# Performance work log

Hardware: AMD Instinct MI355X
Metric: run time of the kernel (lower is better)

The kernel has to match this reference:

```python
import jax, jax.numpy as jnp
import numpy as np

B, T, D, H = 512, 200, 128, 128


def setup_inputs() -> dict:
    key = jax.random.key(0)
    ks = jax.random.split(key, 16)
    r = lambda k, shp, s=0.05: jax.random.normal(k, shp, dtype=jnp.float32) * s
    F = 3 * D + H  # concat([item_eb, his_sum, item_eb*his_sum, final_state2])
    return {
        "item_eb": jax.random.normal(ks[0], (B, D), dtype=jnp.float32),
        "item_his_eb": jax.random.normal(ks[1], (B, T, D), dtype=jnp.float32),
        "Wg1": r(ks[2], (D + H, 2 * H)), "bg1": jnp.ones((2 * H,), jnp.float32),
        "Wc1": r(ks[3], (D + H, H)), "bc1": jnp.zeros((H,), jnp.float32),
        "att_w1": r(ks[4], (4 * H, 80)), "att_b1": jnp.zeros((80,), jnp.float32),
        "att_w2": r(ks[5], (80, 40)), "att_b2": jnp.zeros((40,), jnp.float32),
        "att_w3": r(ks[6], (40, 1)), "att_b3": jnp.zeros((1,), jnp.float32),
        "Wg2": r(ks[7], (2 * H, 2 * H)), "bg2": jnp.ones((2 * H,), jnp.float32),
        "Wc2": r(ks[8], (2 * H, H)), "bc2": jnp.zeros((H,), jnp.float32),
        "fc1_w": r(ks[9], (F, 200)), "fc1_b": jnp.zeros((200,), jnp.float32),
        "alpha1": jnp.full((200,), 0.25, jnp.float32),
        "fc2_w": r(ks[10], (200, 80)), "fc2_b": jnp.zeros((80,), jnp.float32),
        "alpha2": jnp.full((80,), 0.25, jnp.float32),
        "fc3_w": r(ks[11], (80, 2)), "fc3_b": jnp.zeros((2,), jnp.float32),
        "seq_len": jax.random.randint(ks[12], (B,), 1, T + 1).astype(jnp.int32),
    }


def _gru_scan(x_btd, Wg, bg, Wc, bc, seq_len, att=None):
    """GRU (TF GRUCell math) or AUGRU if att [B,T] is given.
    Honors sequence_length semantics of tf dynamic_rnn: state copied through,
    outputs zeroed past each row's length."""
    Bx, Tx, _ = x_btd.shape
    Hh = Wc.shape[1]
    xs = jnp.swapaxes(x_btd, 0, 1)  # [T,B,Din]
    ts = jnp.arange(Tx)
    a_ts = jnp.swapaxes(att, 0, 1) if att is not None else jnp.zeros((Tx, Bx), x_btd.dtype)
    h0 = jnp.zeros((Bx, Hh), x_btd.dtype)

    def step(h, xat):
        x, a, t = xat
        gates = jax.nn.sigmoid(jnp.concatenate([x, h], axis=-1) @ Wg + bg)
        rg, u = jnp.split(gates, 2, axis=-1)
        c = jnp.tanh(jnp.concatenate([x, rg * h], axis=-1) @ Wc + bc)
        if att is not None:  # VecAttGRUCell: u = (1 - att_score) * u
            u = (1.0 - a[:, None]) * u
        hn = u * h + (1.0 - u) * c
        valid = (t < seq_len)[:, None]
        hn = jnp.where(valid, hn, h)
        out = jnp.where(valid, hn, jnp.zeros_like(hn))
        return hn, out

    hT, outs = jax.lax.scan(step, h0, (xs, a_ts, ts))
    return jnp.swapaxes(outs, 0, 1), hT  # [B,T,H], [B,H]


def _forward(item_eb, item_his_eb, Wg1, bg1, Wc1, bc1, att_w1, att_b1, att_w2, att_b2,
             att_w3, att_b3, Wg2, bg2, Wc2, bc2, fc1_w, fc1_b, alpha1, fc2_w, fc2_b,
             alpha2, fc3_w, fc3_b, seq_len):
    Bx, Tx, Dx = item_his_eb.shape
    mask = jnp.arange(Tx)[None, :] < seq_len[:, None]  # [B,T] bool
    # rnn_1: plain GRU over history embeddings
    rnn1, _ = _gru_scan(item_his_eb, Wg1, bg1, Wc1, bc1, seq_len)
    # din_fcn_attention: concat trick + 3-layer scorer + masked softmax
    q = jnp.broadcast_to(item_eb[:, None, :], rnn1.shape)
    din_all = jnp.concatenate([q, rnn1, q - rnn1, q * rnn1], axis=-1)  # [B,T,4H]
    h1 = jax.nn.sigmoid(din_all @ att_w1 + att_b1)
    h2 = jax.nn.sigmoid(h1 @ att_w2 + att_b2)
    scores = (h2 @ att_w3 + att_b3)[..., 0]  # [B,T]
    NEG_INF = jnp.float32(-(2.0 ** 32) + 1.0)  # DIEN padding value
    scores = jnp.where(mask, scores, NEG_INF)
    alphas = jax.nn.softmax(scores, axis=-1)  # [B,T]
    # rnn_2: AUGRU (VecAttGRUCell) gated by attention scores; take final state
    _, final_state2 = _gru_scan(rnn1, Wg2, bg2, Wc2, bc2, seq_len, att=alphas)
    # fcn head on concatenated features
    his_sum = jnp.sum(item_his_eb * mask[..., None].astype(item_his_eb.dtype), axis=1)
    feat = jnp.concatenate([item_eb, his_sum, item_eb * his_sum, final_state2], axis=-1)
    prelu = lambda x, a: jnp.maximum(x, 0.0) + a * jnp.minimum(x, 0.0)
    z = prelu(feat @ fc1_w + fc1_b, alpha1)
    z = prelu(z @ fc2_w + fc2_b, alpha2)
    logits = z @ fc3_w + fc3_b  # [B,2]
    return jax.nn.softmax(logits, axis=-1)


def reference(item_eb, item_his_eb, Wg1, bg1, Wc1, bc1, att_w1, att_b1, att_w2, att_b2,
              att_w3, att_b3, Wg2, bg2, Wc2, bc2, fc1_w, fc1_b, alpha1, fc2_w, fc2_b,
              alpha2, fc3_w, fc3_b, seq_len):
    return _forward(item_eb, item_his_eb, Wg1, bg1, Wc1, bc1, att_w1, att_b1, att_w2,
                    att_b2, att_w3, att_b3, Wg2, bg2, Wc2, bc2, fc1_w, fc1_b, alpha1,
                    fc2_w, fc2_b, alpha2, fc3_w, fc3_b, seq_len)
```

## Files before the change

kernel.cpp:

```cpp
#include <hip/hip_runtime.h>
#include <hip/hip_bf16.h>


typedef __attribute__((ext_vector_type(8))) short bf16x8;
typedef __attribute__((ext_vector_type(4))) float f32x4;
typedef _Float16 f16x2 __attribute__((ext_vector_type(2)));

#define NC 4
#define TC 50

static __device__ __forceinline__ unsigned short f2bf(float f) {
  union { __hip_bfloat16 h; unsigned short u; } v;
  v.h = __float2bfloat16(f);
  return v.u;
}
static __device__ __forceinline__ float bf2f(unsigned short u) {
  union { __hip_bfloat16 h; unsigned short u; } v;
  v.u = u;
  return __bfloat162float(v.h);
}
static __device__ __forceinline__ unsigned short f2h(float f) {
  union { _Float16 h; unsigned short u; } v;
  v.h = (_Float16)f;
  return v.u;
}
static __device__ __forceinline__ unsigned int pkf16(float a, float b) {
  union { f16x2 v; unsigned int u; } c;
  c.v = (f16x2){(_Float16)a, (_Float16)b};
  return c.u;
}
static __device__ __forceinline__ float dot2f(unsigned int w, unsigned int h, float acc) {
  union { unsigned int u; f16x2 v; } a, b;
  a.u = w; b.u = h;
#if __has_builtin(__builtin_amdgcn_fdot2)
  return __builtin_amdgcn_fdot2(a.v, b.v, acc, false);
#else
  return acc + (float)a.v.x * (float)b.v.x + (float)a.v.y * (float)b.v.y;
#endif
}

__global__ __launch_bounds__(256) void prep_weights(
    const float* __restrict__ Wg1, const float* __restrict__ Wc1,
    const float* __restrict__ Wg2, const float* __restrict__ Wc2,
    const float* __restrict__ aw1, const float* __restrict__ aw2,
    const float* __restrict__ bg1, const float* __restrict__ bc1,
    const float* __restrict__ bg2, const float* __restrict__ bc2,
    const float* __restrict__ ab1, const float* __restrict__ ab2,
    unsigned short* __restrict__ W1xT, unsigned short* __restrict__ W2xT,
    unsigned short* __restrict__ AW1T, unsigned short* __restrict__ AW2T,
    float* __restrict__ b384_1, float* __restrict__ b384_2,
    float* __restrict__ bA1, float* __restrict__ bA2,
    unsigned int* __restrict__ WgP1, unsigned int* __restrict__ WcP1,
    unsigned int* __restrict__ WgP2, unsigned int* __restrict__ WcP2)
{
  int e = blockIdx.x * 256 + threadIdx.x;
  if (e < 49152) {
    int n = e >> 7, k = e & 127;
    float v1 = (n < 256) ? Wg1[k * 256 + n] : Wc1[k * 128 + (n - 256)];
    float v2 = (n < 256) ? Wg2[k * 256 + n] : Wc2[k * 128 + (n - 256)];
    W1xT[e] = f2bf(v1);
    W2xT[e] = f2bf(v2);
  }
  if (e < 65536) {
    int n = e >> 9, k = e & 511;
    AW1T[e] = f2bf(n < 80 ? aw1[k * 80 + n] : 0.f);
  }
  if (e < 16384) {
    int n = e >> 7, k = e & 127;
    AW2T[e] = f2bf((n < 40 && k < 80) ? aw2[k * 40 + n] : 0.f);
  }
  if (e < 16384) {
    int i = e >> 8, tt = e & 255;
    int row = 128 + 2 * i;
    WgP1[e] = pkf16(Wg1[row * 256 + tt], Wg1[(row + 1) * 256 + tt]);
    WgP2[e] = pkf16(Wg2[row * 256 + tt], Wg2[(row + 1) * 256 + tt]);
  }
  if (e < 8192) {
    int i = e >> 8, tt = e & 255;
    int jc = tt >> 1, half = tt & 1;
    int row = 128 + half * 64 + 2 * i;
    WcP1[e] = pkf16(Wc1[row * 128 + jc], Wc1[(row + 1) * 128 + jc]);
    WcP2[e] = pkf16(Wc2[row * 128 + jc], Wc2[(row + 1) * 128 + jc]);
  }
  if (e < 384) {
    b384_1[e] = (e < 256) ? bg1[e] : bc1[e - 256];
    b384_2[e] = (e < 256) ? bg2[e] : bc2[e - 256];
  }
  if (e < 128) {
    bA1[e] = (e < 80) ? ab1[e] : 0.f;
    bA2[e] = (e < 40) ? ab2[e] : 0.f;
  }
}

__global__ __launch_bounds__(256) void zero_f(float* __restrict__ p, int n) {
  int i = blockIdx.x * 256 + threadIdx.x;
  if (i < n) p[i] = 0.f;
}

__global__ __launch_bounds__(256) void cast_his_t(const float4* __restrict__ in4,
                                                  ushort4* __restrict__ out4)
{
  int i = blockIdx.x * 256 + threadIdx.x;
  float4 v = in4[i];
  int d4 = (i & 31) << 2;
  int bt = i >> 5;
  int tt = bt % 200, bb = bt / 200;
  out4[(((size_t)tt * 512 + bb) * 128 + d4) >> 2] =
      make_ushort4(f2bf(v.x), f2bf(v.y), f2bf(v.z), f2bf(v.w));
}

template <int EPI>
__global__ __launch_bounds__(256) void gemm_bt(
    const unsigned short* __restrict__ A, const unsigned short* __restrict__ BT,
    const float* __restrict__ bias, float* __restrict__ Cf,
    unsigned short* __restrict__ Cb, int K, int ldc)
{
  __shared__ uint4 AsB[1024];
  __shared__ uint4 BsB[1024];
  const int tid = threadIdx.x;
  const int w = tid >> 6, l = tid & 63;
  const long mBase = (long)blockIdx.x * 128;
  const int nBase = blockIdx.y * 128;

  f32x4 acc[2][8];
#pragma unroll
  for (int m = 0; m < 2; m++)
#pragma unroll
    for (int n = 0; n < 8; n++) acc[m][n] = 0.f;

  const int srow = (tid >> 3) & 31;
  const int scc = l & 7;

  for (int kb = 0; kb < K; kb += 64) {
#pragma unroll
    for (int p = 0; p < 4; p++) {
      int row = p * 32 + srow;
      uint4 va = *(const uint4*)(A + (size_t)(mBase + row) * K + kb + scc * 8);
      uint4 vb = *(const uint4*)(BT + (size_t)(nBase + row) * K + kb + scc * 8);
      AsB[row * 8 + (scc ^ (row & 7))] = va;
      BsB[row * 8 + (scc ^ (row & 7))] = vb;
    }
    __syncthreads();
#pragma unroll
    for (int ks = 0; ks < 2; ks++) {
      int ccr = ks * 4 + (l >> 4);
      int r0 = w * 32 + (l & 15);
      int r1 = r0 + 16;
      bf16x8 a0 = *(const bf16x8*)&AsB[r0 * 8 + (ccr ^ (r0 & 7))];
      bf16x8 a1 = *(const bf16x8*)&AsB[r1 * 8 + (ccr ^ (r1 & 7))];
#pragma unroll
      for (int n = 0; n < 8; n++) {
        int rb = n * 16 + (l & 15);
        bf16x8 bn = *(const bf16x8*)&BsB[rb * 8 + (ccr ^ (rb & 7))];
        acc[0][n] = __builtin_amdgcn_mfma_f32_16x16x32_bf16(a0, bn, acc[0][n], 0, 0, 0);
        acc[1][n] = __builtin_amdgcn_mfma_f32_16x16x32_bf16(a1, bn, acc[1][n], 0, 0, 0);
      }
    }
    __syncthreads();
  }

  const int lcol = l & 15, lrow4 = (l >> 4) * 4;
#pragma unroll
  for (int n = 0; n < 8; n++) {
    int gcol = nBase + n * 16 + lcol;
    float bb = bias[gcol];
#pragma unroll
    for (int m = 0; m < 2; m++) {
#pragma unroll
      for (int i = 0; i < 4; i++) {
        long grow = mBase + w * 32 + m * 16 + lrow4 + i;
        float v = acc[m][n][i] + bb;
        if (EPI == 0) {
          Cf[grow * ldc + gcol] = v;
        } else if (EPI == 1) {
          Cb[grow * ldc + gcol] = f2bf(1.f / (1.f + __expf(-v)));
        } else {
          Cb[grow * ldc + gcol] = f2h(v);
        }
      }
    }
  }
}

template <int AUGRU>
__global__ __launch_bounds__(256, 3) void gru_chunk(
    const unsigned short* __restrict__ xproj,
    const unsigned int* __restrict__ WgP,
    const unsigned int* __restrict__ WcP,
    const int* __restrict__ seqlen,
    const float* __restrict__ alphas,
    unsigned short* __restrict__ outbf,
    float* __restrict__ hstate,
    int tbase)
{
  const int t = threadIdx.x;
  const int r = blockIdx.x;
  const int jc = t >> 1, half = t & 1;
  const int len = seqlen[r];
  int nsteps = len - tbase;
  if (nsteps > TC) nsteps = TC;

  if (nsteps <= 0) {
    if (!AUGRU) {
      for (int s = 0; s < TC; s++) {
        unsigned int* zp = (unsigned int*)(outbf + ((size_t)(tbase + s) * 512 + r) * 128);
        if (t < 64) zp[t] = 0;
      }
    }
    return;
  }

  unsigned int wg[64], wc[32];
#pragma unroll
  for (int i = 0; i < 64; i++) wg[i] = WgP[i * 256 + t];
#pragma unroll
  for (int i = 0; i < 32; i++) wc[i] = WcP[i * 256 + t];

  __shared__ float hF[128];
  __shared__ float uF[128];
  __shared__ unsigned int hH[64];
  __shared__ unsigned int rghP[64];

  if (t < 128) hF[t] = hstate[r * 128 + t];
  if (t < 64) hH[t] = pkf16(hstate[r * 128 + 2 * t], hstate[r * 128 + 2 * t + 1]);
  __syncthreads();

  const _Float16* xp = (const _Float16*)xproj;
  const size_t rowStride = (size_t)512 * 384;
  float xg = (float)xp[(size_t)r * 384 + t];
  float xc = (float)xp[(size_t)r * 384 + 256 + jc];
  float al = AUGRU ? alphas[r * 200 + tbase] : 0.f;

  for (int ts = 0; ts < nsteps; ++ts) {
    float a0 = 0.f, a1 = 0.f, a2 = 0.f, a3 = 0.f;
#pragma unroll
    for (int q = 0; q < 4; q++) {
      uint4 h0 = *(const uint4*)&hH[q * 16 + 0];
      uint4 h1 = *(const uint4*)&hH[q * 16 + 4];
      uint4 h2 = *(const uint4*)&hH[q * 16 + 8];
      uint4 h3 = *(const uint4*)&hH[q * 16 + 12];
      a0 = dot2f(wg[q * 16 + 0], h0.x, a0);  a1 = dot2f(wg[q * 16 + 1], h0.y, a1);
      a2 = dot2f(wg[q * 16 + 2], h0.z, a2);  a3 = dot2f(wg[q * 16 + 3], h0.w, a3);
      a0 = dot2f(wg[q * 16 + 4], h1.x, a0);  a1 = dot2f(wg[q * 16 + 5], h1.y, a1);
      a2 = dot2f(wg[q * 16 + 6], h1.z, a2);  a3 = dot2f(wg[q * 16 + 7], h1.w, a3);
      a0 = dot2f(wg[q * 16 + 8], h2.x, a0);  a1 = dot2f(wg[q * 16 + 9], h2.y, a1);
      a2 = dot2f(wg[q * 16 + 10], h2.z, a2); a3 = dot2f(wg[q * 16 + 11], h2.w, a3);
      a0 = dot2f(wg[q * 16 + 12], h3.x, a0); a1 = dot2f(wg[q * 16 + 13], h3.y, a1);
      a2 = dot2f(wg[q * 16 + 14], h3.z, a2); a3 = dot2f(wg[q * 16 + 15], h3.w, a3);
    }
    float a = (a0 + a1) + (a2 + a3) + xg;
    float g = 1.f / (1.f + __expf(-a));
    float rgh = 0.f;
    if (t < 128) rgh = g * hF[t];
    float rh2 = __shfl_down(rgh, 1);
    if (t < 128) {
      if ((t & 1) == 0) rghP[t >> 1] = pkf16(rgh, rh2);
    } else {
      uF[t - 128] = g;
    }
    int tsn = (ts + 1 < nsteps) ? ts + 1 : nsteps - 1;
    float xg_n = (float)xp[(size_t)tsn * rowStride + (size_t)r * 384 + t];
    float xc_n = (float)xp[(size_t)tsn * rowStride + (size_t)r * 384 + 256 + jc];
    float al_n = AUGRU ? alphas[r * 200 + tbase + tsn] : 0.f;
    __syncthreads();

    float c0 = 0.f, c1 = 0.f;
    const uint4* rp = (const uint4*)&rghP[half * 32];
#pragma unroll
    for (int q = 0; q < 8; q++) {
      uint4 rq = rp[q];
      c0 = dot2f(wc[q * 4 + 0], rq.x, c0);
      c1 = dot2f(wc[q * 4 + 1], rq.y, c1);
      c0 = dot2f(wc[q * 4 + 2], rq.z, c0);
      c1 = dot2f(wc[q * 4 + 3], rq.w, c1);
    }
    float c = c0 + c1;
    c += __shfl_xor(c, 1);
    c += xc;
    c = fminf(fmaxf(c, -15.f), 15.f);
    float e2 = __expf(2.f * c);
    c = 1.f - 2.f / (e2 + 1.f);
    float u = uF[jc];
    if (AUGRU) u *= (1.f - al);
    float h = hF[jc];
    float hn = u * h + (1.f - u) * c;
    float hnHi = __shfl_down(hn, 2);
    if ((t & 1) == 0) {
      hF[jc] = hn;
      if (!AUGRU) outbf[((size_t)(tbase + ts) * 512 + r) * 128 + jc] = f2bf(hn);
    }
    if ((t & 3) == 0) hH[t >> 2] = pkf16(hn, hnHi);
    __syncthreads();

    xg = xg_n; xc = xc_n; al = al_n;
  }

  if (t < 128) hstate[r * 128 + t] = hF[t];
  if (!AUGRU && nsteps < TC) {
    for (int s = nsteps; s < TC; s++) {
      unsigned int* zp = (unsigned int*)(outbf + ((size_t)(tbase + s) * 512 + r) * 128);
      if (t < 64) zp[t] = 0;
    }
  }
}

__global__ __launch_bounds__(256) void build_din(
    const float* __restrict__ item_eb, const unsigned short* __restrict__ rnn1bf,
    ushort4* __restrict__ din, int rowbase)
{
  int i = blockIdx.x * 256 + threadIdx.x;
  int r = i >> 5;
  int d4 = (i & 31) << 2;
  int b = r & 511;
  float4 q = *(const float4*)(item_eb + b * 128 + d4);
  const unsigned short* rp = rnn1bf + ((size_t)rowbase + r) * 128 + d4;
  unsigned short s0 = rp[0], s1 = rp[1], s2 = rp[2], s3 = rp[3];
  float r0 = bf2f(s0), r1 = bf2f(s1), r2 = bf2f(s2), r3 = bf2f(s3);
  size_t base = (size_t)r * 512 + d4;
  din[(base + 0) >> 2]   = make_ushort4(f2bf(q.x), f2bf(q.y), f2bf(q.z), f2bf(q.w));
  din[(base + 128) >> 2] = make_ushort4(s0, s1, s2, s3);
  din[(base + 256) >> 2] = make_ushort4(f2bf(q.x - r0), f2bf(q.y - r1), f2bf(q.z - r2), f2bf(q.w - r3));
  din[(base + 384) >> 2] = make_ushort4(f2bf(q.x * r0), f2bf(q.y * r1), f2bf(q.z * r2), f2bf(q.w * r3));
}

__global__ __launch_bounds__(256) void scorer(
    const unsigned short* __restrict__ h2, const float* __restrict__ w3,
    const float* __restrict__ b3, float* __restrict__ scores, int tbase)
{
  int r = blockIdx.x * 256 + threadIdx.x;
  int b = r & 511, tp = r >> 9;
  const unsigned short* row = h2 + (size_t)r * 128;
  float acc = b3[0];
#pragma unroll 8
  for (int k = 0; k < 40; k++) acc += bf2f(row[k]) * w3[k];
  scores[b * 200 + tbase + tp] = acc;
}

__global__ __launch_bounds__(256) void mask_softmax(
    const float* __restrict__ scores, const int* __restrict__ seqlen,
    float* __restrict__ alphas)
{
  int b = blockIdx.x, t = threadIdx.x;
  __shared__ float red[256];
  int len = seqlen[b];
  float s = (t < 200 && t < len) ? scores[b * 200 + t] : -1e30f;
  red[t] = s;
  __syncthreads();
  for (int o = 128; o > 0; o >>= 1) {
    if (t < o) red[t] = fmaxf(red[t], red[t + o]);
    __syncthreads();
  }
  float m = red[0];
  __syncthreads();
  float e = (t < 200 && t < len) ? __expf(s - m) : 0.f;
  red[t] = e;
  __syncthreads();
  for (int o = 128; o > 0; o >>= 1) {
    if (t < o) red[t] += red[t + o];
    __syncthreads();
  }
  float denom = red[0];
  if (t < 200) alphas[b * 200 + t] = e / denom;
}

__global__ __launch_bounds__(128) void feat_kernel(
    const float* __restrict__ item_eb, const float* __restrict__ his,
    const int* __restrict__ seqlen, const float* __restrict__ hT,
    float* __restrict__ feat)
{
  int b = blockIdx.x, d = threadIdx.x;
  int len = seqlen[b];
  float s = 0.f;
  const float* hp = his + (size_t)b * 200 * 128 + d;
  for (int ts = 0; ts < len; ++ts) s += hp[ts * 128];
  float q = item_eb[b * 128 + d];
  feat[b * 512 + d] = q;
  feat[b * 512 + 128 + d] = s;
  feat[b * 512 + 256 + d] = q * s;
  feat[b * 512 + 384 + d] = hT[b * 128 + d];
}

__global__ __launch_bounds__(256) void head_kernel(
    const float* __restrict__ feat,
    const float* __restrict__ w1, const float* __restrict__ b1, const float* __restrict__ a1,
    const float* __restrict__ w2, const float* __restrict__ b2, const float* __restrict__ a2,
    const float* __restrict__ w3, const float* __restrict__ b3,
    float* __restrict__ out)
{
  int b = blockIdx.x, t = threadIdx.x;
  __shared__ float frow[512];
  __shared__ float z1[200];
  __shared__ float z2[80];
  frow[t] = feat[b * 512 + t];
  frow[256 + t] = feat[b * 512 + 256 + t];
  __syncthreads();
  if (t < 200) {
    float acc = b1[t];
#pragma unroll 8
    for (int k = 0; k < 512; k++) acc += frow[k] * w1[k * 200 + t];
    z1[t] = acc > 0.f ? acc : a1[t] * acc;
  }
  __syncthreads();
  if (t < 80) {
    float acc = b2[t];
#pragma unroll 8
    for (int k = 0; k < 200; k++) acc += z1[k] * w2[k * 80 + t];
    z2[t] = acc > 0.f ? acc : a2[t] * acc;
  }
  __syncthreads();
  if (t == 0) {
    float l0 = b3[0], l1 = b3[1];
    for (int k = 0; k < 80; k++) {
      float z = z2[k];
      l0 += z * w3[k * 2];
      l1 += z * w3[k * 2 + 1];
    }
    float m = fmaxf(l0, l1);
    float e0 = __expf(l0 - m), e1 = __expf(l1 - m);
    out[b * 2 + 0] = e0 / (e0 + e1);
    out[b * 2 + 1] = e1 / (e0 + e1);
  }
}

extern "C" void kernel_launch(void* const* d_in, const int* in_sizes, int n_in,
                              void* d_out, int out_size, void* d_ws, size_t ws_size,
                              hipStream_t stream)
{
  const float* item_eb = (const float*)d_in[0];
  const float* his     = (const float*)d_in[1];
  const float* Wg1     = (const float*)d_in[2];
  const float* bg1     = (const float*)d_in[3];
  const float* Wc1     = (const float*)d_in[4];
  const float* bc1     = (const float*)d_in[5];
  const float* aw1     = (const float*)d_in[6];
  const float* ab1     = (const float*)d_in[7];
  const float* aw2     = (const float*)d_in[8];
  const float* ab2     = (const float*)d_in[9];
  const float* aw3     = (const float*)d_in[10];
  const float* ab3     = (const float*)d_in[11];
  const float* Wg2     = (const float*)d_in[12];
  const float* bg2     = (const float*)d_in[13];
  const float* Wc2     = (const float*)d_in[14];
  const float* bc2     = (const float*)d_in[15];
  const float* fc1w    = (const float*)d_in[16];
  const float* fc1b    = (const float*)d_in[17];
  const float* al1     = (const float*)d_in[18];
  const float* fc2w    = (const float*)d_in[19];
  const float* fc2b    = (const float*)d_in[20];
  const float* al2     = (const float*)d_in[21];
  const float* fc3w    = (const float*)d_in[22];
  const float* fc3b    = (const float*)d_in[23];
  const int*   seqlen  = (const int*)d_in[24];

  char* ws = (char*)d_ws;
  unsigned short* XhA    = (unsigned short*)(ws + 0L);
  unsigned short* xprojC = (unsigned short*)(ws + 26214400L);
  unsigned short* h1C    = (unsigned short*)(ws + 26214400L);
  unsigned short* h2C    = (unsigned short*)(ws + 32768000L);
  unsigned short* rnn1   = (unsigned short*)(ws + 45875200L);
  float*          scores = (float*)(ws + 72089600L);
  float*          alphas = (float*)(ws + 72499200L);
  float*          hstate = (float*)(ws + 72908800L);
  float*          feat   = (float*)(ws + 73170944L);
  unsigned int*   WgP1   = (unsigned int*)(ws + 74219520L);
  unsigned int*   WcP1   = (unsigned int*)(ws + 74285056L);
  unsigned int*   WgP2   = (unsigned int*)(ws + 74317824L);
  unsigned int*   WcP2   = (unsigned int*)(ws + 74383360L);
  unsigned short* W1xT   = (unsigned short*)(ws + 74416128L);
  unsigned short* W2xT   = (unsigned short*)(ws + 74514432L);
  unsigned short* AW1T   = (unsigned short*)(ws + 74612736L);
  unsigned short* AW2T   = (unsigned short*)(ws + 74743808L);
  float*          b384_1 = (float*)(ws + 74776576L);
  float*          b384_2 = (float*)(ws + 74778112L);
  float*          bA1    = (float*)(ws + 74779648L);
  float*          bA2    = (float*)(ws + 74780160L);

  const size_t chunkRows = (size_t)TC * 512;

  prep_weights<<<256, 256, 0, stream>>>(Wg1, Wc1, Wg2, Wc2, aw1, aw2, bg1, bc1,
                                        bg2, bc2, ab1, ab2,
                                        W1xT, W2xT, AW1T, AW2T, b384_1, b384_2, bA1, bA2,
                                        WgP1, WcP1, WgP2, WcP2);
  cast_his_t<<<12800, 256, 0, stream>>>((const float4*)his, (ushort4*)XhA);
  zero_f<<<256, 256, 0, stream>>>(hstate, 65536);

  for (int c = 0; c < NC; c++) {
    gemm_bt<2><<<dim3(200, 3), 256, 0, stream>>>(XhA + c * chunkRows * 128, W1xT,
                                                 b384_1, nullptr, xprojC, 128, 384);
    gru_chunk<0><<<512, 256, 0, stream>>>(xprojC, WgP1, WcP1, seqlen, nullptr,
                                          rnn1, hstate, c * TC);
  }

  for (int c = 0; c < NC; c++) {
    build_din<<<3200, 256, 0, stream>>>(item_eb, rnn1, (ushort4*)XhA, (int)(c * chunkRows));
    gemm_bt<1><<<dim3(200, 1), 256, 0, stream>>>(XhA, AW1T, bA1, nullptr, h1C, 512, 128);
    gemm_bt<1><<<dim3(200, 1), 256, 0, stream>>>(h1C, AW2T, bA2, nullptr, h2C, 128, 128);
    scorer<<<100, 256, 0, stream>>>(h2C, aw3, ab3, scores, c * TC);
  }
  mask_softmax<<<512, 256, 0, stream>>>(scores, seqlen, alphas);

  zero_f<<<256, 256, 0, stream>>>(hstate, 65536);
  for (int c = 0; c < NC; c++) {
    gemm_bt<2><<<dim3(200, 3), 256, 0, stream>>>(rnn1 + c * chunkRows * 128, W2xT,
                                                 b384_2, nullptr, xprojC, 128, 384);
    gru_chunk<1><<<512, 256, 0, stream>>>(xprojC, WgP2, WcP2, seqlen, alphas,
                                          nullptr, hstate, c * TC);
  }

  feat_kernel<<<512, 128, 0, stream>>>(item_eb, his, seqlen, hstate, feat);
  head_kernel<<<512, 256, 0, stream>>>(feat, fc1w, fc1b, al1, fc2w, fc2b, al2,
                                       fc3w, fc3b, (float*)d_out);
}
```

Baseline: 744.2 us.

## Fuse GRU chunks with next-chunk projection and attention GEMMs in combined launches

```diff
diff --git a/kernel.cpp b/kernel.cpp
--- a/kernel.cpp
+++ b/kernel.cpp
@@ -8,6 +8,8 @@
 
 #define NC 4
 #define TC 50
+#define CROWS 25600
+#define CSH 3276800
 
 static __device__ __forceinline__ unsigned short f2bf(float f) {
   union { __hip_bfloat16 h; unsigned short u; } v;
@@ -24,25 +26,26 @@
   v.h = (_Float16)f;
   return v.u;
 }
+static __device__ __forceinline__ float h2f(unsigned short u) {
+  union { unsigned short u; _Float16 h; } v;
+  v.u = u;
+  return (float)v.h;
+}
 static __device__ __forceinline__ unsigned int pkf16(float a, float b) {
   union { f16x2 v; unsigned int u; } c;
   c.v = (f16x2){(_Float16)a, (_Float16)b};
   return c.u;
 }
-static __device__ __forceinline__ float dot2f(unsigned int w, unsigned int h, float acc) {
-  union { unsigned int u; f16x2 v; } a, b;
-  a.u = w; b.u = h;
-#if __has_builtin(__builtin_amdgcn_fdot2)
-  return __builtin_amdgcn_fdot2(a.v, b.v, acc, false);
-#else
-  return acc + (float)a.v.x * (float)b.v.x + (float)a.v.y * (float)b.v.y;
-#endif
+static __device__ __forceinline__ void dot2a(float& acc, unsigned int w, unsigned int h) {
+  asm volatile("v_dot2_f32_f16 %0, %1, %2, %0" : "+v"(acc) : "v"(w), "v"(h));
 }
 
 __global__ __launch_bounds__(256) void prep_weights(
+    const float* __restrict__ item_eb,
     const float* __restrict__ Wg1, const float* __restrict__ Wc1,
     const float* __restrict__ Wg2, const float* __restrict__ Wc2,
     const float* __restrict__ aw1, const float* __restrict__ aw2,
+    const float* __restrict__ aw3,
     const float* __restrict__ bg1, const float* __restrict__ bc1,
     const float* __restrict__ bg2, const float* __restrict__ bc2,
     const float* __restrict__ ab1, const float* __restrict__ ab2,
@@ -51,7 +54,9 @@
     float* __restrict__ b384_1, float* __restrict__ b384_2,
     float* __restrict__ bA1, float* __restrict__ bA2,
     unsigned int* __restrict__ WgP1, unsigned int* __restrict__ WcP1,
-    unsigned int* __restrict__ WgP2, unsigned int* __restrict__ WcP2)
+    unsigned int* __restrict__ WgP2, unsigned int* __restrict__ WcP2,
+    float* __restrict__ w3p, unsigned short* __restrict__ Xq,
+    float* __restrict__ hstate)
 {
   int e = blockIdx.x * 256 + threadIdx.x;
   if (e < 49152) {
@@ -64,6 +69,8 @@
   if (e < 65536) {
     int n = e >> 9, k = e & 511;
     AW1T[e] = f2bf(n < 80 ? aw1[k * 80 + n] : 0.f);
+    Xq[e] = f2bf(item_eb[e]);
+    hstate[e] = 0.f;
   }
   if (e < 16384) {
     int n = e >> 7, k = e & 127;
@@ -89,12 +96,8 @@
   if (e < 128) {
     bA1[e] = (e < 80) ? ab1[e] : 0.f;
     bA2[e] = (e < 40) ? ab2[e] : 0.f;
-  }
-}
-
-__global__ __launch_bounds__(256) void zero_f(float* __restrict__ p, int n) {
-  int i = blockIdx.x * 256 + threadIdx.x;
-  if (i < n) p[i] = 0.f;
+    w3p[e] = (e < 40) ? aw3[e] : 0.f;
+  }
 }
 
 __global__ __launch_bounds__(256) void cast_his_t(const float4* __restrict__ in4,
@@ -109,18 +112,42 @@
       make_ushort4(f2bf(v.x), f2bf(v.y), f2bf(v.z), f2bf(v.w));
 }
 
-template <int EPI>
-__global__ __launch_bounds__(256) void gemm_bt(
-    const unsigned short* __restrict__ A, const unsigned short* __restrict__ BT,
-    const float* __restrict__ bias, float* __restrict__ Cf,
-    unsigned short* __restrict__ Cb, int K, int ldc)
-{
-  __shared__ uint4 AsB[1024];
-  __shared__ uint4 BsB[1024];
+struct GemmP {
+  const unsigned short* A;
+  const unsigned short* B;
+  const float* bias;
+  unsigned short* out;
+  float* scores;
+  const float* w3p;
+  const float* b3;
+  const unsigned short* Xq;
+  const unsigned short* rnn1;
+  long rowbase;
+  int K, ldc, mtiles, tbase;
+};
+
+static __device__ __forceinline__ uint4 bfop(uint4 q, uint4 r, bool mul) {
+  unsigned short* qs = (unsigned short*)&q;
+  unsigned short* rs = (unsigned short*)&r;
+  uint4 o;
+  unsigned short* os = (unsigned short*)&o;
+#pragma unroll
+  for (int i = 0; i < 8; i++) {
+    float a = bf2f(qs[i]), b = bf2f(rs[i]);
+    os[i] = f2bf(mul ? a * b : a - b);
+  }
+  return o;
+}
+
+template <int SRC, int EPI>
+__device__ __forceinline__ void gemm_body(const GemmP& P, int tile, char* smem) {
+  uint4* AsB = (uint4*)smem;
+  uint4* BsB = AsB + 1024;
   const int tid = threadIdx.x;
   const int w = tid >> 6, l = tid & 63;
-  const long mBase = (long)blockIdx.x * 128;
-  const int nBase = blockIdx.y * 128;
+  const int mb = tile % P.mtiles, nb = tile / P.mtiles;
+  const long mBase = (long)mb * 128;
+  const int nBase = nb * 128;
 
   f32x4 acc[2][8];
 #pragma unroll
@@ -130,13 +157,31 @@
 
   const int srow = (tid >> 3) & 31;
   const int scc = l & 7;
-
-  for (int kb = 0; kb < K; kb += 64) {
+  const int KK = SRC ? 512 : P.K;
+
+  for (int kb = 0; kb < KK; kb += 64) {
 #pragma unroll
     for (int p = 0; p < 4; p++) {
       int row = p * 32 + srow;
-      uint4 va = *(const uint4*)(A + (size_t)(mBase + row) * K + kb + scc * 8);
-      uint4 vb = *(const uint4*)(BT + (size_t)(nBase + row) * K + kb + scc * 8);
+      long grow = mBase + row;
+      uint4 va;
+      if (SRC == 0) {
+        va = *(const uint4*)(P.A + (size_t)grow * KK + kb + scc * 8);
+      } else {
+        int seg = kb >> 7;
+        int c0 = (kb & 127) + scc * 8;
+        int b = (int)(grow & 511);
+        if (seg == 0) {
+          va = *(const uint4*)(P.Xq + b * 128 + c0);
+        } else if (seg == 1) {
+          va = *(const uint4*)(P.rnn1 + (size_t)(P.rowbase + grow) * 128 + c0);
+        } else {
+          uint4 vq = *(const uint4*)(P.Xq + b * 128 + c0);
+          uint4 vr = *(const uint4*)(P.rnn1 + (size_t)(P.rowbase + grow) * 128 + c0);
+          va = bfop(vq, vr, seg == 3);
+        }
+      }
+      uint4 vb = *(const uint4*)(P.B + (size_t)(nBase + row) * KK + kb + scc * 8);
       AsB[row * 8 + (scc ^ (row & 7))] = va;
       BsB[row * 8 + (scc ^ (row & 7))] = vb;
     }
@@ -160,78 +205,115 @@
   }
 
   const int lcol = l & 15, lrow4 = (l >> 4) * 4;
-#pragma unroll
-  for (int n = 0; n < 8; n++) {
-    int gcol = nBase + n * 16 + lcol;
-    float bb = bias[gcol];
-#pragma unroll
-    for (int m = 0; m < 2; m++) {
-#pragma unroll
-      for (int i = 0; i < 4; i++) {
-        long grow = mBase + w * 32 + m * 16 + lrow4 + i;
-        float v = acc[m][n][i] + bb;
-        if (EPI == 0) {
-          Cf[grow * ldc + gcol] = v;
-        } else if (EPI == 1) {
-          Cb[grow * ldc + gcol] = f2bf(1.f / (1.f + __expf(-v)));
-        } else {
-          Cb[grow * ldc + gcol] = f2h(v);
+  if (EPI == 2) {
+    float sp[2][4] = {{0.f, 0.f, 0.f, 0.f}, {0.f, 0.f, 0.f, 0.f}};
+#pragma unroll
+    for (int n = 0; n < 8; n++) {
+      int gcol = n * 16 + lcol;
+      float bb = P.bias[gcol];
+      float w3 = P.w3p[gcol];
+#pragma unroll
+      for (int m = 0; m < 2; m++)
+#pragma unroll
+        for (int i = 0; i < 4; i++) {
+          float v = acc[m][n][i] + bb;
+          sp[m][i] += w3 / (1.f + __expf(-v));
         }
-      }
-    }
-  }
-}
+    }
+#pragma unroll
+    for (int msk = 1; msk < 16; msk <<= 1)
+#pragma unroll
+      for (int m = 0; m < 2; m++)
+#pragma unroll
+        for (int i = 0; i < 4; i++) sp[m][i] += __shfl_xor(sp[m][i], msk);
+    float b3v = P.b3[0];
+    if (lcol == 0) {
+#pragma unroll
+      for (int m = 0; m < 2; m++)
+#pragma unroll
+        for (int i = 0; i < 4; i++) {
+          long grow = mBase + w * 32 + m * 16 + lrow4 + i;
+          int b = (int)(grow & 511);
+          int tp = (int)(grow >> 9) + P.tbase;
+          P.scores[b * 200 + tp] = sp[m][i] + b3v;
+        }
+    }
+  } else {
+#pragma unroll
+    for (int n = 0; n < 8; n++) {
+      int gcol = nBase + n * 16 + lcol;
+      float bb = P.bias[gcol];
+#pragma unroll
+      for (int m = 0; m < 2; m++)
+#pragma unroll
+        for (int i = 0; i < 4; i++) {
+          long grow = mBase + w * 32 + m * 16 + lrow4 + i;
+          float v = acc[m][n][i] + bb;
+          if (EPI == 0) P.out[grow * P.ldc + gcol] = f2h(v);
+          else          P.out[grow * P.ldc + gcol] = f2bf(1.f / (1.f + __expf(-v)));
+        }
+    }
+  }
+}
+
+struct GruP {
+  const unsigned short* xproj;
+  const unsigned int* WgP;
+  const unsigned int* WcP;
+  const int* seqlen;
+  const float* alphas;
+  unsigned short* outbf;
+  float* hstate;
+  int tbase;
+};
 
 template <int AUGRU>
-__global__ __launch_bounds__(256, 3) void gru_chunk(
-    const unsigned short* __restrict__ xproj,
-    const unsigned int* __restrict__ WgP,
-    const unsigned int* __restrict__ WcP,
-    const int* __restrict__ seqlen,
-    const float* __restrict__ alphas,
-    unsigned short* __restrict__ outbf,
-    float* __restrict__ hstate,
-    int tbase)
-{
+__device__ void gru_body(const GruP& P, int r, char* smem) {
+  float* hF = (float*)smem;
+  float* uF = hF + 128;
+  unsigned int* hH = (unsigned int*)(uF + 128);
+  unsigned int* rghP = hH + 64;
   const int t = threadIdx.x;
-  const int r = blockIdx.x;
-  const int jc = t >> 1, half = t & 1;
-  const int len = seqlen[r];
-  int nsteps = len - tbase;
+  const int jc = t >> 1;
+  const int len = P.seqlen[r];
+  int nsteps = len - P.tbase;
   if (nsteps > TC) nsteps = TC;
 
   if (nsteps <= 0) {
-    if (!AUGRU) {
-      for (int s = 0; s < TC; s++) {
-        unsigned int* zp = (unsigned int*)(outbf + ((size_t)(tbase + s) * 512 + r) * 128);
-        if (t < 64) zp[t] = 0;
-      }
+    if (!AUGRU && t < 64) {
+      for (int s = 0; s < TC; s++)
+        ((unsigned int*)(P.outbf + ((size_t)(P.tbase + s) * 512 + r) * 128))[t] = 0;
     }
     return;
   }
+  __builtin_amdgcn_s_setprio(1);
 
   unsigned int wg[64], wc[32];
 #pragma unroll
-  for (int i = 0; i < 64; i++) wg[i] = WgP[i * 256 + t];
-#pragma unroll
-  for (int i = 0; i < 32; i++) wc[i] = WcP[i * 256 + t];
-
-  __shared__ float hF[128];
-  __shared__ float uF[128];
-  __shared__ unsigned int hH[64];
-  __shared__ unsigned int rghP[64];
-
-  if (t < 128) hF[t] = hstate[r * 128 + t];
-  if (t < 64) hH[t] = pkf16(hstate[r * 128 + 2 * t], hstate[r * 128 + 2 * t + 1]);
-  __syncthreads();
-
-  const _Float16* xp = (const _Float16*)xproj;
-  const size_t rowStride = (size_t)512 * 384;
-  float xg = (float)xp[(size_t)r * 384 + t];
-  float xc = (float)xp[(size_t)r * 384 + 256 + jc];
-  float al = AUGRU ? alphas[r * 200 + tbase] : 0.f;
+  for (int i = 0; i < 64; i++) wg[i] = P.WgP[i * 256 + t];
+#pragma unroll
+  for (int i = 0; i < 32; i++) wc[i] = P.WcP[i * 256 + t];
+
+  if (t < 128) hF[t] = P.hstate[r * 128 + t];
+  if (t < 64) hH[t] = pkf16(P.hstate[r * 128 + 2 * t], P.hstate[r * 128 + 2 * t + 1]);
+  __syncthreads();
+
+  const unsigned short* xp = P.xproj;
+  const size_t RS = (size_t)512 * 384;
+  const size_t base = (size_t)r * 384;
+  unsigned short gA = xp[base + t], cA = xp[base + 256 + jc];
+  int s1 = nsteps > 1 ? 1 : 0;
+  unsigned short gB = xp[s1 * RS + base + t], cB = xp[s1 * RS + base + 256 + jc];
+  float alA = AUGRU ? P.alphas[r * 200 + P.tbase] : 0.f;
+  float alB = AUGRU ? P.alphas[r * 200 + P.tbase + s1] : 0.f;
 
   for (int ts = 0; ts < nsteps; ++ts) {
+    int tsn = (ts + 2 < nsteps) ? ts + 2 : nsteps - 1;
+    size_t off = (size_t)tsn * RS + base;
+    unsigned short gC = xp[off + t];
+    unsigned short cC = xp[off + 256 + jc];
+    float alC = AUGRU ? P.alphas[r * 200 + P.tbase + tsn] : 0.f;
+
     float a0 = 0.f, a1 = 0.f, a2 = 0.f, a3 = 0.f;
 #pragma unroll
     for (int q = 0; q < 4; q++) {
@@ -239,109 +321,93 @@
       uint4 h1 = *(const uint4*)&hH[q * 16 + 4];
       uint4 h2 = *(const uint4*)&hH[q * 16 + 8];
       uint4 h3 = *(const uint4*)&hH[q * 16 + 12];
-      a0 = dot2f(wg[q * 16 + 0], h0.x, a0);  a1 = dot2f(wg[q * 16 + 1], h0.y, a1);
-      a2 = dot2f(wg[q * 16 + 2], h0.z, a2);  a3 = dot2f(wg[q * 16 + 3], h0.w, a3);
-      a0 = dot2f(wg[q * 16 + 4], h1.x, a0);  a1 = dot2f(wg[q * 16 + 5], h1.y, a1);
-      a2 = dot2f(wg[q * 16 + 6], h1.z, a2);  a3 = dot2f(wg[q * 16 + 7], h1.w, a3);
-      a0 = dot2f(wg[q * 16 + 8], h2.x, a0);  a1 = dot2f(wg[q * 16 + 9], h2.y, a1);
-      a2 = dot2f(wg[q * 16 + 10], h2.z, a2); a3 = dot2f(wg[q * 16 + 11], h2.w, a3);
-      a0 = dot2f(wg[q * 16 + 12], h3.x, a0); a1 = dot2f(wg[q * 16 + 13], h3.y, a1);
-      a2 = dot2f(wg[q * 16 + 14], h3.z, a2); a3 = dot2f(wg[q * 16 + 15], h3.w, a3);
-    }
-    float a = (a0 + a1) + (a2 + a3) + xg;
+      dot2a(a0, wg[q * 16 + 0], h0.x);  dot2a(a1, wg[q * 16 + 1], h0.y);
+      dot2a(a2, wg[q * 16 + 2], h0.z);  dot2a(a3, wg[q * 16 + 3], h0.w);
+      dot2a(a0, wg[q * 16 + 4], h1.x);  dot2a(a1, wg[q * 16 + 5], h1.y);
+      dot2a(a2, wg[q * 16 + 6], h1.z);  dot2a(a3, wg[q * 16 + 7], h1.w);
+      dot2a(a0, wg[q * 16 + 8], h2.x);  dot2a(a1, wg[q * 16 + 9], h2.y);
+      dot2a(a2, wg[q * 16 + 10], h2.z); dot2a(a3, wg[q * 16 + 11], h2.w);
+      dot2a(a0, wg[q * 16 + 12], h3.x); dot2a(a1, wg[q * 16 + 13], h3.y);
+      dot2a(a2, wg[q * 16 + 14], h3.z); dot2a(a3, wg[q * 16 + 15], h3.w);
+    }
+    float a = (a0 + a1) + (a2 + a3) + h2f(gA);
     float g = 1.f / (1.f + __expf(-a));
-    float rgh = 0.f;
-    if (t < 128) rgh = g * hF[t];
-    float rh2 = __shfl_down(rgh, 1);
     if (t < 128) {
-      if ((t & 1) == 0) rghP[t >> 1] = pkf16(rgh, rh2);
+      float rgh = g * hF[t];
+      float rh2 = __shfl_down(rgh, 1);
+      if (!(t & 1)) rghP[t >> 1] = pkf16(rgh, rh2);
     } else {
       uF[t - 128] = g;
     }
-    int tsn = (ts + 1 < nsteps) ? ts + 1 : nsteps - 1;
-    float xg_n = (float)xp[(size_t)tsn * rowStride + (size_t)r * 384 + t];
-    float xc_n = (float)xp[(size_t)tsn * rowStride + (size_t)r * 384 + 256 + jc];
-    float al_n = AUGRU ? alphas[r * 200 + tbase + tsn] : 0.f;
     __syncthreads();
 
     float c0 = 0.f, c1 = 0.f;
-    const uint4* rp = (const uint4*)&rghP[half * 32];
+    const uint4* rp = (const uint4*)&rghP[(t & 1) * 32];
 #pragma unroll
     for (int q = 0; q < 8; q++) {
       uint4 rq = rp[q];
-      c0 = dot2f(wc[q * 4 + 0], rq.x, c0);
-      c1 = dot2f(wc[q * 4 + 1], rq.y, c1);
-      c0 = dot2f(wc[q * 4 + 2], rq.z, c0);
-      c1 = dot2f(wc[q * 4 + 3], rq.w, c1);
+      dot2a(c0, wc[q * 4 + 0], rq.x);
+      dot2a(c1, wc[q * 4 + 1], rq.y);
+      dot2a(c0, wc[q * 4 + 2], rq.z);
+      dot2a(c1, wc[q * 4 + 3], rq.w);
     }
     float c = c0 + c1;
     c += __shfl_xor(c, 1);
-    c += xc;
+    c += h2f(cA);
     c = fminf(fmaxf(c, -15.f), 15.f);
     float e2 = __expf(2.f * c);
     c = 1.f - 2.f / (e2 + 1.f);
     float u = uF[jc];
-    if (AUGRU) u *= (1.f - al);
+    if (AUGRU) u *= (1.f - alA);
     float h = hF[jc];
     float hn = u * h + (1.f - u) * c;
     float hnHi = __shfl_down(hn, 2);
-    if ((t & 1) == 0) {
+    if (!(t & 1)) {
       hF[jc] = hn;
-      if (!AUGRU) outbf[((size_t)(tbase + ts) * 512 + r) * 128 + jc] = f2bf(hn);
-    }
-    if ((t & 3) == 0) hH[t >> 2] = pkf16(hn, hnHi);
+      if (!AUGRU) P.outbf[((size_t)(P.tbase + ts) * 512 + r) * 128 + jc] = f2bf(hn);
+    }
+    if (!(t & 3)) hH[t >> 2] = pkf16(hn, hnHi);
     __syncthreads();
 
-    xg = xg_n; xc = xc_n; al = al_n;
-  }
-
-  if (t < 128) hstate[r * 128 + t] = hF[t];
-  if (!AUGRU && nsteps < TC) {
-    for (int s = nsteps; s < TC; s++) {
-      unsigned int* zp = (unsigned int*)(outbf + ((size_t)(tbase + s) * 512 + r) * 128);
-      if (t < 64) zp[t] = 0;
-    }
-  }
-}
-
-__global__ __launch_bounds__(256) void build_din(
-    const float* __restrict__ item_eb, const unsigned short* __restrict__ rnn1bf,
-    ushort4* __restrict__ din, int rowbase)
+    gA = gB; cA = cB; alA = alB;
+    gB = gC; cB = cC; alB = alC;
+  }
+
+  if (t < 128) P.hstate[r * 128 + t] = hF[t];
+  if (!AUGRU && nsteps < TC && t < 64) {
+    for (int s = nsteps; s < TC; s++)
+      ((unsigned int*)(P.outbf + ((size_t)(P.tbase + s) * 512 + r) * 128))[t] = 0;
+  }
+}
+
+template <int AUG, int GRU, int S1, int E1, int S2, int E2, int S3, int E3>
+__global__ __launch_bounds__(256) void fatk(GruP gp, GemmP p1, int c1,
+                                            GemmP p2, int c2, GemmP p3)
 {
-  int i = blockIdx.x * 256 + threadIdx.x;
-  int r = i >> 5;
-  int d4 = (i & 31) << 2;
-  int b = r & 511;
-  float4 q = *(const float4*)(item_eb + b * 128 + d4);
-  const unsigned short* rp = rnn1bf + ((size_t)rowbase + r) * 128 + d4;
-  unsigned short s0 = rp[0], s1 = rp[1], s2 = rp[2], s3 = rp[3];
-  float r0 = bf2f(s0), r1 = bf2f(s1), r2 = bf2f(s2), r3 = bf2f(s3);
-  size_t base = (size_t)r * 512 + d4;
-  din[(base + 0) >> 2]   = make_ushort4(f2bf(q.x), f2bf(q.y), f2bf(q.z), f2bf(q.w));
-  din[(base + 128) >> 2] = make_ushort4(s0, s1, s2, s3);
-  din[(base + 256) >> 2] = make_ushort4(f2bf(q.x - r0), f2bf(q.y - r1), f2bf(q.z - r2), f2bf(q.w - r3));
-  din[(base + 384) >> 2] = make_ushort4(f2bf(q.x * r0), f2bf(q.y * r1), f2bf(q.z * r2), f2bf(q.w * r3));
-}
-
-__global__ __launch_bounds__(256) void scorer(
-    const unsigned short* __restrict__ h2, const float* __restrict__ w3,
-    const float* __restrict__ b3, float* __restrict__ scores, int tbase)
-{
-  int r = blockIdx.x * 256 + threadIdx.x;
-  int b = r & 511, tp = r >> 9;
-  const unsigned short* row = h2 + (size_t)r * 128;
-  float acc = b3[0];
-#pragma unroll 8
-  for (int k = 0; k < 40; k++) acc += bf2f(row[k]) * w3[k];
-  scores[b * 200 + tbase + tp] = acc;
+  extern __shared__ char smem[];
+  int id = blockIdx.x;
+  if constexpr (GRU) {
+    if (id < 512) { gru_body<AUG>(gp, id, smem); return; }
+    id -= 512;
+  }
+  if constexpr (S1 >= 0) {
+    if (id < c1) { gemm_body<S1, E1>(p1, id, smem); return; }
+    id -= c1;
+  }
+  if constexpr (S2 >= 0) {
+    if (id < c2) { gemm_body<S2, E2>(p2, id, smem); return; }
+    id -= c2;
+  }
+  if constexpr (S3 >= 0) gemm_body<S3, E3>(p3, id, smem);
 }
 
 __global__ __launch_bounds__(256) void mask_softmax(
     const float* __restrict__ scores, const int* __restrict__ seqlen,
-    float* __restrict__ alphas)
+    float* __restrict__ alphas, float* __restrict__ hstate)
 {
   int b = blockIdx.x, t = threadIdx.x;
   __shared__ float red[256];
+  if (t < 128) hstate[b * 128 + t] = 0.f;
   int len = seqlen[b];
   float s = (t < 200 && t < len) ? scores[b * 200 + t] : -1e30f;
   red[t] = s;
@@ -363,25 +429,9 @@
   if (t < 200) alphas[b * 200 + t] = e / denom;
 }
 
-__global__ __launch_bounds__(128) void feat_kernel(
+__global__ __launch_bounds__(256) void head_kernel(
     const float* __restrict__ item_eb, const float* __restrict__ his,
-    const int* __restrict__ seqlen, const float* __restrict__ hT,
-    float* __restrict__ feat)
-{
-  int b = blockIdx.x, d = threadIdx.x;
-  int len = seqlen[b];
-  float s = 0.f;
-  const float* hp = his + (size_t)b * 200 * 128 + d;
-  for (int ts = 0; ts < len; ++ts) s += hp[ts * 128];
-  float q = item_eb[b * 128 + d];
-  feat[b * 512 + d] = q;
-  feat[b * 512 + 128 + d] = s;
-  feat[b * 512 + 256 + d] = q * s;
-  feat[b * 512 + 384 + d] = hT[b * 128 + d];
-}
-
-__global__ __launch_bounds__(256) void head_kernel(
-    const float* __restrict__ feat,
+    const int* __restrict__ seqlen, const float* __restrict__ hstate,
     const float* __restrict__ w1, const float* __restrict__ b1, const float* __restrict__ a1,
     const float* __restrict__ w2, const float* __restrict__ b2, const float* __restrict__ a2,
     const float* __restrict__ w3, const float* __restrict__ b3,
@@ -391,8 +441,21 @@
   __shared__ float frow[512];
   __shared__ float z1[200];
   __shared__ float z2[80];
-  frow[t] = feat[b * 512 + t];
-  frow[256 + t] = feat[b * 512 + 256 + t];
+  __shared__ float hs2[256];
+  int len = seqlen[b];
+  int col = t & 127, hf = t >> 7;
+  float s = 0.f;
+  for (int ts = hf; ts < len; ts += 2) s += his[((size_t)b * 200 + ts) * 128 + col];
+  hs2[t] = s;
+  __syncthreads();
+  if (t < 128) {
+    float sv = hs2[t] + hs2[t + 128];
+    float q = item_eb[b * 128 + t];
+    frow[t] = q;
+    frow[128 + t] = sv;
+    frow[256 + t] = q * sv;
+    frow[384 + t] = hstate[b * 128 + t];
+  }
   __syncthreads();
   if (t < 200) {
     float acc = b1[t];
@@ -454,60 +517,87 @@
 
   char* ws = (char*)d_ws;
   unsigned short* XhA    = (unsigned short*)(ws + 0L);
-  unsigned short* xprojC = (unsigned short*)(ws + 26214400L);
-  unsigned short* h1C    = (unsigned short*)(ws + 26214400L);
-  unsigned short* h2C    = (unsigned short*)(ws + 32768000L);
-  unsigned short* rnn1   = (unsigned short*)(ws + 45875200L);
-  float*          scores = (float*)(ws + 72089600L);
-  float*          alphas = (float*)(ws + 72499200L);
-  float*          hstate = (float*)(ws + 72908800L);
-  float*          feat   = (float*)(ws + 73170944L);
-  unsigned int*   WgP1   = (unsigned int*)(ws + 74219520L);
-  unsigned int*   WcP1   = (unsigned int*)(ws + 74285056L);
-  unsigned int*   WgP2   = (unsigned int*)(ws + 74317824L);
-  unsigned int*   WcP2   = (unsigned int*)(ws + 74383360L);
-  unsigned short* W1xT   = (unsigned short*)(ws + 74416128L);
-  unsigned short* W2xT   = (unsigned short*)(ws + 74514432L);
-  unsigned short* AW1T   = (unsigned short*)(ws + 74612736L);
-  unsigned short* AW2T   = (unsigned short*)(ws + 74743808L);
-  float*          b384_1 = (float*)(ws + 74776576L);
-  float*          b384_2 = (float*)(ws + 74778112L);
-  float*          bA1    = (float*)(ws + 74779648L);
-  float*          bA2    = (float*)(ws + 74780160L);
-
-  const size_t chunkRows = (size_t)TC * 512;
-
-  prep_weights<<<256, 256, 0, stream>>>(Wg1, Wc1, Wg2, Wc2, aw1, aw2, bg1, bc1,
-                                        bg2, bc2, ab1, ab2,
+  unsigned short* xpA    = (unsigned short*)(ws + 26214400L);
+  unsigned short* xpB    = (unsigned short*)(ws + 45875200L);
+  unsigned short* rnn1   = (unsigned short*)(ws + 65536000L);
+  float*          scores = (float*)(ws + 91750400L);
+  float*          alphas = (float*)(ws + 92160000L);
+  float*          hstate = (float*)(ws + 92569600L);
+  unsigned int*   WgP1   = (unsigned int*)(ws + 92831744L);
+  unsigned int*   WcP1   = (unsigned int*)(ws + 92897280L);
+  unsigned int*   WgP2   = (unsigned int*)(ws + 92930048L);
+  unsigned int*   WcP2   = (unsigned int*)(ws + 92995584L);
+  unsigned short* W1xT   = (unsigned short*)(ws + 93028352L);
+  unsigned short* W2xT   = (unsigned short*)(ws + 93126656L);
+  unsigned short* AW1T   = (unsigned short*)(ws + 93224960L);
+  unsigned short* AW2T   = (unsigned short*)(ws + 93356032L);
+  float*          b384_1 = (float*)(ws + 93388800L);
+  float*          b384_2 = (float*)(ws + 93390336L);
+  float*          bA1    = (float*)(ws + 93391872L);
+  float*          bA2    = (float*)(ws + 93392384L);
+  float*          w3p    = (float*)(ws + 93392896L);
+  unsigned short* Xq     = (unsigned short*)(ws + 93393408L);
+
+  unsigned short* h1[NC] = {XhA, XhA + CSH, XhA + 2 * CSH, XhA + 3 * CSH};
+
+  const int SM = 32768;
+  GruP gz{}; GemmP dz{};
+
+  auto mkGru = [&](int c, int aug) {
+    GruP g;
+    g.xproj = (c & 1) ? xpB : xpA;
+    g.WgP = aug ? WgP2 : WgP1; g.WcP = aug ? WcP2 : WcP1;
+    g.seqlen = seqlen; g.alphas = alphas;
+    g.outbf = aug ? nullptr : rnn1; g.hstate = hstate; g.tbase = c * TC;
+    return g;
+  };
+  auto mkXp = [&](const unsigned short* A, const float* bias, unsigned short* outp) {
+    GemmP p{}; p.A = A; p.B = (bias == b384_1) ? W1xT : W2xT; p.bias = bias;
+    p.out = outp; p.K = 128; p.ldc = 384; p.mtiles = 200; return p;
+  };
+  auto mkAtt1 = [&](int c) {
+    GemmP p{}; p.B = AW1T; p.bias = bA1; p.out = h1[c];
+    p.Xq = Xq; p.rnn1 = rnn1; p.rowbase = (long)c * CROWS;
+    p.K = 512; p.ldc = 128; p.mtiles = 200; return p;
+  };
+  auto mkAtt2 = [&](int c) {
+    GemmP p{}; p.A = h1[c]; p.B = AW2T; p.bias = bA2;
+    p.scores = scores; p.w3p = w3p; p.b3 = ab3;
+    p.K = 128; p.ldc = 128; p.mtiles = 200; p.tbase = c * TC; return p;
+  };
+
+  prep_weights<<<256, 256, 0, stream>>>(item_eb, Wg1, Wc1, Wg2, Wc2, aw1, aw2, aw3,
+                                        bg1, bc1, bg2, bc2, ab1, ab2,
                                         W1xT, W2xT, AW1T, AW2T, b384_1, b384_2, bA1, bA2,
-                                        WgP1, WcP1, WgP2, WcP2);
+                                        WgP1, WcP1, WgP2, WcP2, w3p, Xq, hstate);
   cast_his_t<<<12800, 256, 0, stream>>>((const float4*)his, (ushort4*)XhA);
-  zero_f<<<256, 256, 0, stream>>>(hstate, 65536);
-
-  for (int c = 0; c < NC; c++) {
-    gemm_bt<2><<<dim3(200, 3), 256, 0, stream>>>(XhA + c * chunkRows * 128, W1xT,
-                                                 b384_1, nullptr, xprojC, 128, 384);
-    gru_chunk<0><<<512, 256, 0, stream>>>(xprojC, WgP1, WcP1, seqlen, nullptr,
-                                          rnn1, hstate, c * TC);
-  }
-
-  for (int c = 0; c < NC; c++) {
-    build_din<<<3200, 256, 0, stream>>>(item_eb, rnn1, (ushort4*)XhA, (int)(c * chunkRows));
-    gemm_bt<1><<<dim3(200, 1), 256, 0, stream>>>(XhA, AW1T, bA1, nullptr, h1C, 512, 128);
-    gemm_bt<1><<<dim3(200, 1), 256, 0, stream>>>(h1C, AW2T, bA2, nullptr, h2C, 128, 128);
-    scorer<<<100, 256, 0, stream>>>(h2C, aw3, ab3, scores, c * TC);
-  }
-  mask_softmax<<<512, 256, 0, stream>>>(scores, seqlen, alphas);
-
-  zero_f<<<256, 256, 0, stream>>>(hstate, 65536);
-  for (int c = 0; c < NC; c++) {
-    gemm_bt<2><<<dim3(200, 3), 256, 0, stream>>>(rnn1 + c * chunkRows * 128, W2xT,
-                                                 b384_2, nullptr, xprojC, 128, 384);
-    gru_chunk<1><<<512, 256, 0, stream>>>(xprojC, WgP2, WcP2, seqlen, alphas,
-                                          nullptr, hstate, c * TC);
-  }
-
-  feat_kernel<<<512, 128, 0, stream>>>(item_eb, his, seqlen, hstate, feat);
-  head_kernel<<<512, 256, 0, stream>>>(feat, fc1w, fc1b, al1, fc2w, fc2b, al2,
+
+  fatk<0,0, 0,0, -1,0, -1,0><<<600, 256, SM, stream>>>(
+      gz, mkXp(XhA, b384_1, xpA), 600, dz, 0, dz);
+  fatk<0,1, 0,0, -1,0, -1,0><<<1112, 256, SM, stream>>>(
+      mkGru(0,0), mkXp(XhA + (size_t)CSH, b384_1, xpB), 600, dz, 0, dz);
+  fatk<0,1, 0,0, -1,0, -1,0><<<1112, 256, SM, stream>>>(
+      mkGru(1,0), mkXp(XhA + (size_t)2*CSH, b384_1, xpA), 600, dz, 0, dz);
+  fatk<0,1, 0,0, 1,1, -1,0><<<1712, 256, SM, stream>>>(
+      mkGru(2,0), mkXp(XhA + (size_t)3*CSH, b384_1, xpB), 600, mkAtt1(0), 200, dz);
+  fatk<0,1, 1,1, 0,2, -1,0><<<912, 256, SM, stream>>>(
+      mkGru(3,0), mkAtt1(1), 200, mkAtt2(0), 200, dz);
+  fatk<0,0, 1,1, 0,2, 0,0><<<1000, 256, SM, stream>>>(
+      gz, mkAtt1(2), 200, mkAtt2(1), 200, mkXp(rnn1, b384_2, xpA));
+  fatk<0,0, 1,1, 0,2, 0,0><<<1000, 256, SM, stream>>>(
+      gz, mkAtt1(3), 200, mkAtt2(2), 200, mkXp(rnn1 + (size_t)CSH, b384_2, xpB));
+  fatk<0,0, 0,2, -1,0, -1,0><<<200, 256, SM, stream>>>(
+      gz, mkAtt2(3), 200, dz, 0, dz);
+  mask_softmax<<<512, 256, 0, stream>>>(scores, seqlen, alphas, hstate);
+  fatk<1,1, -1,0, -1,0, -1,0><<<512, 256, SM, stream>>>(
+      mkGru(0,1), dz, 0, dz, 0, dz);
+  fatk<1,1, 0,0, -1,0, -1,0><<<1112, 256, SM, stream>>>(
+      mkGru(1,1), mkXp(rnn1 + (size_t)2*CSH, b384_2, xpA), 600, dz, 0, dz);
+  fatk<1,1, 0,0, -1,0, -1,0><<<1112, 256, SM, stream>>>(
+      mkGru(2,1), mkXp(rnn1 + (size_t)3*CSH, b384_2, xpB), 600, dz, 0, dz);
+  fatk<1,1, -1,0, -1,0, -1,0><<<512, 256, SM, stream>>>(
+      mkGru(3,1), dz, 0, dz, 0, dz);
+  head_kernel<<<512, 256, 0, stream>>>(item_eb, his, seqlen, hstate,
+                                       fc1w, fc1b, al1, fc2w, fc2b, al2,
                                        fc3w, fc3b, (float*)d_out);
 }
```

Measured after the change: 677.4 us. 9.0% less time.
